# Optimization experiments

Measured on AMD Instinct MI355X. Metric: run time of the kernel, lower is better.

Reference implementation:

```python
import jax, jax.numpy as jnp
import numpy as np

# Conv config matching init_kwargs
C_IN, C_OUT = 128, 256
KH, KW = 3, 3
STRIDE = (1, 1)
PADDING = ((1, 1), (1, 1))
DILATION = (1, 1)
B, H, W = 32, 56, 56


def setup_inputs() -> dict:
    key = jax.random.key(0)
    k1, k2, k3 = jax.random.split(key, 3)
    x = jax.random.normal(k1, (B, C_IN, H, W), dtype=jnp.float32)
    # Flattened weight as stored by Conv2DUF: conv.weight.view(O,-1).t() -> [C*kh*kw, O]
    weight = jax.random.normal(k2, (C_IN * KH * KW, C_OUT), dtype=jnp.float32) * 0.02
    bias = jax.random.normal(k3, (C_OUT,), dtype=jnp.float32) * 0.02
    return {"x": x, "weight": weight, "bias": bias}


def reference(x, weight, bias):
    # Conv2DUF computes unfold(x) @ weight + bias, which is exactly a 2D
    # cross-correlation with the original conv kernel. Recover the [O,C,kh,kw]
    # kernel from the flattened [C*kh*kw, O] matrix and use the fused conv
    # primitive (same math, no giant im2col buffer).
    kernel = weight.T.reshape(C_OUT, C_IN, KH, KW)
    out = jax.lax.conv_general_dilated(
        x, kernel,
        window_strides=STRIDE,
        padding=PADDING,
        rhs_dilation=DILATION,
        dimension_numbers=("NCHW", "OIHW", "NCHW"),
    )
    return out + bias[None, :, None, None]
```

## Files before the change

kernel.cpp:

```cpp
#include <hip/hip_runtime.h>
#include <stdint.h>


#define C_INQ 128
#define C_OUTQ 256
#define HDIM 56
#define WDIM 56
#define BDIM 32
#define HP 58
#define WP 58
#define HWPIX (HDIM * WDIM)
#define GSTRIDE (BDIM * HP * WP * 8)
#define XT_ELEMS ((size_t)16 * GSTRIDE)
#define XT_BYTES (XT_ELEMS * 2)

typedef __bf16 bf16x8 __attribute__((ext_vector_type(8)));
typedef unsigned short ushort8 __attribute__((ext_vector_type(8)));
typedef float floatx4 __attribute__((ext_vector_type(4)));

__device__ __forceinline__ unsigned short f2bf(float f) {
  union { float f; unsigned int u; } v; v.f = f;
  unsigned int u = v.u;
  unsigned int r = u + 0x7FFFu + ((u >> 16) & 1u);
  return (unsigned short)(r >> 16);
}
__device__ __forceinline__ unsigned int pack2(float a, float b) {
  return (unsigned int)f2bf(a) | ((unsigned int)f2bf(b) << 16);
}

#define PAD_BLOCKS (BDIM * HP)
__global__ __launch_bounds__(256) void prep_kernel(
    const float* __restrict__ x, unsigned short* __restrict__ xt,
    const float* __restrict__ w, unsigned short* __restrict__ wt) {
  const int t = threadIdx.x;
  if (blockIdx.x < PAD_BLOCKS) {
    const int blk = blockIdx.x;
    const int b = blk / HP;
    const int hp = blk - b * HP;
    uint4* __restrict__ xt4 = (uint4*)xt;
    if (hp == 0 || hp == HP - 1) {
      for (int i = t; i < 16 * WP; i += 256) {
        int g = i / WP, wp = i - g * WP;
        xt4[((size_t)(g * BDIM + b) * HP + hp) * WP + wp] = make_uint4(0, 0, 0, 0);
      }
      return;
    }
    const int h = hp - 1;
    if (t < 224) {
      const int g = t / 14;
      const int w4 = (t - g * 14) * 4;
      const float* xp = x + ((size_t)b * C_INQ + g * 8) * HWPIX + h * WDIM + w4;
      float4 L0 = *(const float4*)(xp);
      float4 L1 = *(const float4*)(xp + HWPIX);
      float4 L2 = *(const float4*)(xp + 2 * HWPIX);
      float4 L3 = *(const float4*)(xp + 3 * HWPIX);
      float4 L4 = *(const float4*)(xp + 4 * HWPIX);
      float4 L5 = *(const float4*)(xp + 5 * HWPIX);
      float4 L6 = *(const float4*)(xp + 6 * HWPIX);
      float4 L7 = *(const float4*)(xp + 7 * HWPIX);
      uint4* dst = xt4 + ((size_t)(g * BDIM + b) * HP + hp) * WP + 1 + w4;
      dst[0] = make_uint4(pack2(L0.x, L1.x), pack2(L2.x, L3.x),
                          pack2(L4.x, L5.x), pack2(L6.x, L7.x));
      dst[1] = make_uint4(pack2(L0.y, L1.y), pack2(L2.y, L3.y),
                          pack2(L4.y, L5.y), pack2(L6.y, L7.y));
      dst[2] = make_uint4(pack2(L0.z, L1.z), pack2(L2.z, L3.z),
                          pack2(L4.z, L5.z), pack2(L6.z, L7.z));
      dst[3] = make_uint4(pack2(L0.w, L1.w), pack2(L2.w, L3.w),
                          pack2(L4.w, L5.w), pack2(L6.w, L7.w));
    } else {
      const int r = t - 224;
      const int g = r >> 1;
      const int wp = (r & 1) * (WP - 1);
      xt4[((size_t)(g * BDIM + b) * HP + hp) * WP + wp] = make_uint4(0, 0, 0, 0);
    }
  } else {
    const int bx = blockIdx.x - PAD_BLOCKS;
    const int khw = bx >> 4;
    const int r4 = bx & 15;
    const int n0w = (r4 >> 2) * 64;
    const int c32 = (r4 & 3) * 32;
    __shared__ float lds[32 * 66];
#pragma unroll
    for (int r = 0; r < 8; ++r) {
      int idx = r * 256 + t;
      int n = idx & 63, c = idx >> 6;
      lds[c * 66 + n] = w[(size_t)((c32 + c) * 9 + khw) * C_OUTQ + n0w + n];
    }
    __syncthreads();
    {
      int n = t >> 2, c8 = (t & 3) * 8;
      const float* s = lds + c8 * 66 + n;
      uint4 o;
      o.x = pack2(s[0],   s[66]);
      o.y = pack2(s[132], s[198]);
      o.z = pack2(s[264], s[330]);
      o.w = pack2(s[396], s[462]);
      *(uint4*)(wt + (size_t)khw * (C_OUTQ * C_INQ) + (size_t)(n0w + n) * C_INQ + c32 + c8) = o;
    }
  }
}

#define REGG 352
#define AGRAN (16 * REGG)
#define NTILE 18

__global__ __launch_bounds__(512, 2) void conv_gemm_kernel(
    const unsigned short* __restrict__ xt,
    const unsigned short* __restrict__ wt,
    const float* __restrict__ bias,
    float* __restrict__ out) {
  __shared__ __align__(16) unsigned short ldsA[AGRAN * 8];
  __shared__ __align__(16) unsigned short ldsB[2 * 2048 * 8];

  const int t = threadIdx.x;
  const int lane = t & 63;
  const int wave = t >> 6;
  const int bid = ((int)blockIdx.x & 7) * 56 + ((int)blockIdx.x >> 3);
  const int b = bid / 14;
  const int ht = bid - b * 14;
  const int hp0 = ht * 4;

  int gbaseB[4];
#pragma unroll
  for (int r = 0; r < 4; ++r) {
    int g = r * 512 + t;
    int row = g >> 3;
    int kp = (g & 7) ^ (row & 7);
    gbaseB[r] = row * C_INQ + kp * 8;
  }

  const int wm = (wave >> 2) * 112;
  const int wn = (wave & 3) * 64;
  const int mrow = lane & 15;
  const int quad = lane >> 4;
  const int kxor = mrow & 7;
  const int kx0 = (quad ^ kxor) * 8;
  const int kx1 = ((4 + quad) ^ kxor) * 8;

  int agb[7];
#pragma unroll
  for (int i = 0; i < 7; ++i) {
    int m = wm + i * 16 + mrow;
    int lh = m / 56;
    int w = m - lh * 56;
    agb[i] = quad * REGG + lh * 58 + w;
  }
  int bbase[4];
#pragma unroll
  for (int j = 0; j < 4; ++j) bbase[j] = (wn + j * 16 + mrow) * 64;

  floatx4 acc[7][4] = {};

#pragma unroll
  for (int r = 0; r < 11; ++r) {
    int G = r * 512 + t;
    int gi = G / REGG;
    int q = G - gi * REGG;
    if (q >= 6 * 58) q = 0;
    const unsigned short* src =
        xt + ((size_t)(gi * BDIM + b) * (HP * WP) + hp0 * WP + q) * 8;
    __builtin_amdgcn_global_load_lds(
        (const __attribute__((address_space(1))) unsigned int*)src,
        (__attribute__((address_space(3))) unsigned int*)(ldsA + G * 8),
        16, 0, 0);
  }

  auto stageB = [&](int kt) {
    const int khw = kt >> 1, ch = kt & 1;
    const int koff = khw * (C_OUTQ * C_INQ) + ch * 64;
    unsigned short* base = ldsB + (kt & 1) * 16384;
#pragma unroll
    for (int r = 0; r < 4; ++r)
      __builtin_amdgcn_global_load_lds(
          (const __attribute__((address_space(1))) unsigned int*)(wt + gbaseB[r] + koff),
          (__attribute__((address_space(3))) unsigned int*)(base + r * 4096 + t * 8),
          16, 0, 0);
  };

  stageB(0);
  stageB(1);

#define BC8(p) __builtin_bit_cast(bf16x8, *(const ushort8*)(p))

  auto compute = [&](int kt) {
    const int khw = kt >> 1, ch = kt & 1;
    const int kh = khw / 3, kw = khw - kh * 3;
    const int kadd0 = ch * (8 * REGG) + kh * 58 + kw;
    const unsigned short* Bb = ldsB + (kt & 1) * 16384;
    bf16x8 bfr[4][2];
#pragma unroll
    for (int j = 0; j < 4; ++j) {
      bfr[j][0] = BC8(Bb + bbase[j] + kx0);
      bfr[j][1] = BC8(Bb + bbase[j] + kx1);
    }
    __builtin_amdgcn_s_setprio(1);
#pragma unroll
    for (int i = 0; i < 7; ++i) {
      bf16x8 a0 = BC8(ldsA + (agb[i] + kadd0) * 8);
      bf16x8 a1 = BC8(ldsA + (agb[i] + kadd0 + 4 * REGG) * 8);
#pragma unroll
      for (int j = 0; j < 4; ++j)
        acc[i][j] = __builtin_amdgcn_mfma_f32_16x16x32_bf16(a0, bfr[j][0], acc[i][j], 0, 0, 0);
#pragma unroll
      for (int j = 0; j < 4; ++j)
        acc[i][j] = __builtin_amdgcn_mfma_f32_16x16x32_bf16(a1, bfr[j][1], acc[i][j], 0, 0, 0);
    }
    __builtin_amdgcn_s_setprio(0);
  };

#define K_STEP(KT, VM, DOSTAGE)                                      \
  {                                                                  \
    asm volatile("s_waitcnt vmcnt(" VM ")" ::: "memory");            \
    __builtin_amdgcn_s_barrier();                                    \
    compute(KT);                                                     \
    __builtin_amdgcn_s_barrier();                                    \
    if (DOSTAGE) stageB((KT) + 2);                                   \
  }

#pragma unroll 1
  for (int tt = 0; tt < 16; tt += 2) {
    K_STEP(tt, "4", true);
    K_STEP(tt + 1, "4", true);
  }
  K_STEP(16, "4", false);
  K_STEP(17, "0", false);
#undef K_STEP
#undef BC8

  float bv[4];
#pragma unroll
  for (int j = 0; j < 4; ++j) bv[j] = bias[wn + j * 16 + mrow];
  float* ob = out + (size_t)b * (C_OUTQ * HWPIX) + ht * 224;
#pragma unroll
  for (int i = 0; i < 7; ++i) {
    const int mloc = wm + i * 16 + quad * 4;
#pragma unroll
    for (int j = 0; j < 4; ++j) {
      const int n = wn + j * 16 + mrow;
      floatx4 v = acc[i][j];
      v[0] += bv[j]; v[1] += bv[j]; v[2] += bv[j]; v[3] += bv[j];
      *(floatx4*)(ob + (size_t)n * HWPIX + mloc) = v;
    }
  }
}

extern "C" void kernel_launch(void* const* d_in, const int* in_sizes, int n_in,
                              void* d_out, int out_size, void* d_ws, size_t ws_size,
                              hipStream_t stream) {
  const float* x    = (const float*)d_in[0];
  const float* w    = (const float*)d_in[1];
  const float* bias = (const float*)d_in[2];
  float* out = (float*)d_out;

  unsigned short* xt = (unsigned short*)d_ws;
  unsigned short* wt = (unsigned short*)((char*)d_ws + XT_BYTES);

  hipLaunchKernelGGL(prep_kernel, dim3(PAD_BLOCKS + 144), dim3(256), 0, stream,
                     x, xt, w, wt);
  hipLaunchKernelGGL(conv_gemm_kernel, dim3(448), dim3(512), 0, stream,
                     xt, wt, bias, out);
}
```

Before: 212.8 us.

## Shrink conv tile to two rows and load weight fragments directly from global

The GEMM block tile shrinks from 4 output rows × 256 channels with 8 waves to 2 output rows × 256 channels with 4 waves, so twice as many blocks launch. The LDS double buffer for weights is removed. Each wave now reads its B fragments straight from global memory into registers, double-buffered in registers across K steps, and the per-step barriers are dropped. This removes LDS traffic and synchronisation for B. In exchange, weight reads from global/L2 roughly double, and those loads are no longer swizzled or shared across waves.

```diff
diff --git a/kernel.cpp b/kernel.cpp
--- a/kernel.cpp
+++ b/kernel.cpp
@@ -100,63 +100,30 @@
   }
 }
 
-#define REGG 352
-#define AGRAN (16 * REGG)
-#define NTILE 18
-
-__global__ __launch_bounds__(512, 2) void conv_gemm_kernel(
+#define REG2 240
+#define AG2 (16 * REG2)
+
+__global__ __launch_bounds__(256, 2) void conv_gemm_kernel(
     const unsigned short* __restrict__ xt,
     const unsigned short* __restrict__ wt,
     const float* __restrict__ bias,
     float* __restrict__ out) {
-  __shared__ __align__(16) unsigned short ldsA[AGRAN * 8];
-  __shared__ __align__(16) unsigned short ldsB[2 * 2048 * 8];
+  __shared__ __align__(16) unsigned short ldsA[AG2 * 8];
 
   const int t = threadIdx.x;
   const int lane = t & 63;
   const int wave = t >> 6;
-  const int bid = ((int)blockIdx.x & 7) * 56 + ((int)blockIdx.x >> 3);
-  const int b = bid / 14;
-  const int ht = bid - b * 14;
-  const int hp0 = ht * 4;
-
-  int gbaseB[4];
-#pragma unroll
-  for (int r = 0; r < 4; ++r) {
-    int g = r * 512 + t;
-    int row = g >> 3;
-    int kp = (g & 7) ^ (row & 7);
-    gbaseB[r] = row * C_INQ + kp * 8;
-  }
-
-  const int wm = (wave >> 2) * 112;
-  const int wn = (wave & 3) * 64;
-  const int mrow = lane & 15;
-  const int quad = lane >> 4;
-  const int kxor = mrow & 7;
-  const int kx0 = (quad ^ kxor) * 8;
-  const int kx1 = ((4 + quad) ^ kxor) * 8;
-
-  int agb[7];
-#pragma unroll
-  for (int i = 0; i < 7; ++i) {
-    int m = wm + i * 16 + mrow;
-    int lh = m / 56;
-    int w = m - lh * 56;
-    agb[i] = quad * REGG + lh * 58 + w;
-  }
-  int bbase[4];
-#pragma unroll
-  for (int j = 0; j < 4; ++j) bbase[j] = (wn + j * 16 + mrow) * 64;
-
-  floatx4 acc[7][4] = {};
-
-#pragma unroll
-  for (int r = 0; r < 11; ++r) {
-    int G = r * 512 + t;
-    int gi = G / REGG;
-    int q = G - gi * REGG;
-    if (q >= 6 * 58) q = 0;
+  const int bid = ((int)blockIdx.x & 7) * 112 + ((int)blockIdx.x >> 3);
+  const int b = bid / 28;
+  const int ht = bid - b * 28;
+  const int hp0 = ht * 2;
+
+#pragma unroll
+  for (int r = 0; r < 15; ++r) {
+    int G = r * 256 + t;
+    int gi = G / REG2;
+    int q = G - gi * REG2;
+    if (q >= 4 * 58) q = 0;
     const unsigned short* src =
         xt + ((size_t)(gi * BDIM + b) * (HP * WP) + hp0 * WP + q) * 8;
     __builtin_amdgcn_global_load_lds(
@@ -165,75 +132,84 @@
         16, 0, 0);
   }
 
-  auto stageB = [&](int kt) {
-    const int khw = kt >> 1, ch = kt & 1;
-    const int koff = khw * (C_OUTQ * C_INQ) + ch * 64;
-    unsigned short* base = ldsB + (kt & 1) * 16384;
-#pragma unroll
-    for (int r = 0; r < 4; ++r)
-      __builtin_amdgcn_global_load_lds(
-          (const __attribute__((address_space(1))) unsigned int*)(wt + gbaseB[r] + koff),
-          (__attribute__((address_space(3))) unsigned int*)(base + r * 4096 + t * 8),
-          16, 0, 0);
-  };
-
-  stageB(0);
-  stageB(1);
+  const int wn = wave * 64;
+  const int mrow = lane & 15;
+  const int quad = lane >> 4;
+
+  int agb[7];
+#pragma unroll
+  for (int i = 0; i < 7; ++i) {
+    int m = i * 16 + mrow;
+    int lh = m / 56;
+    int w = m - lh * 56;
+    agb[i] = quad * REG2 + lh * 58 + w;
+  }
+  const unsigned short* bptr[4];
+#pragma unroll
+  for (int j = 0; j < 4; ++j)
+    bptr[j] = wt + (wn + j * 16 + mrow) * C_INQ + quad * 8;
+
+  float bv[4];
+#pragma unroll
+  for (int j = 0; j < 4; ++j) bv[j] = bias[wn + j * 16 + mrow];
+
+  floatx4 acc[7][4] = {};
 
 #define BC8(p) __builtin_bit_cast(bf16x8, *(const ushort8*)(p))
 
-  auto compute = [&](int kt) {
-    const int khw = kt >> 1, ch = kt & 1;
-    const int kh = khw / 3, kw = khw - kh * 3;
-    const int kadd0 = ch * (8 * REGG) + kh * 58 + kw;
-    const unsigned short* Bb = ldsB + (kt & 1) * 16384;
-    bf16x8 bfr[4][2];
-#pragma unroll
-    for (int j = 0; j < 4; ++j) {
-      bfr[j][0] = BC8(Bb + bbase[j] + kx0);
-      bfr[j][1] = BC8(Bb + bbase[j] + kx1);
-    }
-    __builtin_amdgcn_s_setprio(1);
-#pragma unroll
-    for (int i = 0; i < 7; ++i) {
-      bf16x8 a0 = BC8(ldsA + (agb[i] + kadd0) * 8);
-      bf16x8 a1 = BC8(ldsA + (agb[i] + kadd0 + 4 * REGG) * 8);
-#pragma unroll
-      for (int j = 0; j < 4; ++j)
-        acc[i][j] = __builtin_amdgcn_mfma_f32_16x16x32_bf16(a0, bfr[j][0], acc[i][j], 0, 0, 0);
-#pragma unroll
-      for (int j = 0; j < 4; ++j)
-        acc[i][j] = __builtin_amdgcn_mfma_f32_16x16x32_bf16(a1, bfr[j][1], acc[i][j], 0, 0, 0);
-    }
-    __builtin_amdgcn_s_setprio(0);
-  };
-
-#define K_STEP(KT, VM, DOSTAGE)                                      \
-  {                                                                  \
-    asm volatile("s_waitcnt vmcnt(" VM ")" ::: "memory");            \
-    __builtin_amdgcn_s_barrier();                                    \
-    compute(KT);                                                     \
-    __builtin_amdgcn_s_barrier();                                    \
-    if (DOSTAGE) stageB((KT) + 2);                                   \
-  }
+  bf16x8 bA[4][2], bB[4][2];
+#define LOADB(dst, KT)                                                    \
+  {                                                                       \
+    const int khw_ = (KT) >> 1, ch_ = (KT) & 1;                           \
+    const int off_ = khw_ * (C_OUTQ * C_INQ) + ch_ * 64;                  \
+    _Pragma("unroll")                                                     \
+    for (int j = 0; j < 4; ++j) {                                         \
+      dst[j][0] = BC8(bptr[j] + off_);                                    \
+      dst[j][1] = BC8(bptr[j] + off_ + 32);                               \
+    }                                                                     \
+  }
+
+#define COMPUTE(bf, KT)                                                   \
+  {                                                                       \
+    const int khw_ = (KT) >> 1, ch_ = (KT) & 1;                           \
+    const int kh_ = khw_ / 3, kw_ = khw_ - kh_ * 3;                       \
+    const int kadd_ = ch_ * (8 * REG2) + kh_ * 58 + kw_;                  \
+    __builtin_amdgcn_s_setprio(1);                                        \
+    _Pragma("unroll")                                                     \
+    for (int i = 0; i < 7; ++i) {                                         \
+      bf16x8 a0 = BC8(ldsA + (agb[i] + kadd_) * 8);                       \
+      bf16x8 a1 = BC8(ldsA + (agb[i] + kadd_ + 4 * REG2) * 8);            \
+      _Pragma("unroll")                                                   \
+      for (int j = 0; j < 4; ++j)                                         \
+        acc[i][j] = __builtin_amdgcn_mfma_f32_16x16x32_bf16(              \
+            a0, bf[j][0], acc[i][j], 0, 0, 0);                            \
+      _Pragma("unroll")                                                   \
+      for (int j = 0; j < 4; ++j)                                         \
+        acc[i][j] = __builtin_amdgcn_mfma_f32_16x16x32_bf16(              \
+            a1, bf[j][1], acc[i][j], 0, 0, 0);                            \
+    }                                                                     \
+    __builtin_amdgcn_s_setprio(0);                                        \
+  }
+
+  LOADB(bA, 0);
+  __syncthreads();
 
 #pragma unroll 1
-  for (int tt = 0; tt < 16; tt += 2) {
-    K_STEP(tt, "4", true);
-    K_STEP(tt + 1, "4", true);
-  }
-  K_STEP(16, "4", false);
-  K_STEP(17, "0", false);
-#undef K_STEP
+  for (int khw = 0; khw < 9; ++khw) {
+    const int kt = khw * 2;
+    LOADB(bB, kt + 1);
+    COMPUTE(bA, kt);
+    if (khw < 8) LOADB(bA, kt + 2);
+    COMPUTE(bB, kt + 1);
+  }
+#undef LOADB
+#undef COMPUTE
 #undef BC8
 
-  float bv[4];
-#pragma unroll
-  for (int j = 0; j < 4; ++j) bv[j] = bias[wn + j * 16 + mrow];
-  float* ob = out + (size_t)b * (C_OUTQ * HWPIX) + ht * 224;
+  float* ob = out + (size_t)b * (C_OUTQ * HWPIX) + ht * 112;
 #pragma unroll
   for (int i = 0; i < 7; ++i) {
-    const int mloc = wm + i * 16 + quad * 4;
+    const int mloc = i * 16 + quad * 4;
 #pragma unroll
     for (int j = 0; j < 4; ++j) {
       const int n = wn + j * 16 + mrow;
@@ -257,6 +233,6 @@
 
   hipLaunchKernelGGL(prep_kernel, dim3(PAD_BLOCKS + 144), dim3(256), 0, stream,
                      x, xt, w, wt);
-  hipLaunchKernelGGL(conv_gemm_kernel, dim3(448), dim3(512), 0, stream,
+  hipLaunchKernelGGL(conv_gemm_kernel, dim3(896), dim3(256), 0, stream,
                      xt, wt, bias, out);
 }
```

After: 224.9 us. 1.06x slower.
